# Kernel tuning notes

Measured on AMD Instinct MI355X. Metric: run time of the kernel, lower is better.

## Reference

```python
import jax, jax.numpy as jnp
import numpy as np

E = 1024; H = 16; D = E // H; MAX_LEN = 512; B = 4; N = 1024
EPS = 1e-5
NEG_INF = float('-inf')


def layernorm(x, g, b):
    mu = jnp.mean(x, axis=-1, keepdims=True)
    var = jnp.mean((x - mu) ** 2, axis=-1, keepdims=True)
    return (x - mu) * jax.lax.rsqrt(var + EPS) * g + b


def rel_bias(seq_len, rel_pos):
    # rel_pos: (H, MAX_LEN). bias[h,i,j] = rel_pos[h, i-j] if 0<=i-j<MAX_LEN else -inf
    pos = jnp.arange(seq_len)
    rel = pos[:, None] - pos[None, :]                     # (N, N)
    valid = (rel >= 0) & (rel < rel_pos.shape[-1])
    idx = jnp.clip(rel, 0, rel_pos.shape[-1] - 1)
    gathered = rel_pos[:, idx]                            # (H, N, N)
    return jnp.where(valid[None], gathered, NEG_INF)


def setup_inputs() -> dict:
    key = jax.random.key(0)
    ks = jax.random.split(key, 12)
    s = 0.02
    return {
        'x': jax.random.normal(ks[0], (B, N, E), jnp.float32),
        'rel_pos': jax.random.normal(ks[1], (H, MAX_LEN), jnp.float32),
        'in_proj_w': jax.random.normal(ks[2], (3 * E, E), jnp.float32) * s,
        'in_proj_b': jnp.zeros((3 * E,), jnp.float32),
        'out_w': jax.random.normal(ks[3], (E, E), jnp.float32) * s,
        'out_b': jnp.zeros((E,), jnp.float32),
        'w1': jax.random.normal(ks[4], (4 * E, E), jnp.float32) * s,
        'b1': jnp.zeros((4 * E,), jnp.float32),
        'w2': jax.random.normal(ks[5], (E, 4 * E), jnp.float32) * s,
        'b2': jnp.zeros((E,), jnp.float32),
        'ln1_g': jnp.ones((E,), jnp.float32),
        'ln1_b': jnp.zeros((E,), jnp.float32),
        'ln2_g': jnp.ones((E,), jnp.float32),
        'ln2_b': jnp.zeros((E,), jnp.float32),
    }


def reference(x, rel_pos, in_proj_w, in_proj_b, out_w, out_b,
              w1, b1, w2, b2, ln1_g, ln1_b, ln2_g, ln2_b):
    b, n, e = x.shape
    xn = layernorm(x, ln1_g, ln1_b)
    qkv = xn @ in_proj_w.T + in_proj_b                    # (B, N, 3E)
    q, k, v = jnp.split(qkv, 3, axis=-1)
    # (B, N, E) -> (B, H, N, D)
    def heads(t):
        return t.reshape(b, n, H, D).transpose(0, 2, 1, 3)
    q, k, v = heads(q), heads(k), heads(v)
    bias = rel_bias(n, rel_pos)                           # (H, N, N)
    scores = jnp.einsum('bhnd,bhmd->bhnm', q, k) / np.sqrt(D) + bias[None]
    attn = jax.nn.softmax(scores, axis=-1)
    o = jnp.einsum('bhnm,bhmd->bhnd', attn, v)            # (B, H, N, D)
    o = o.transpose(0, 2, 1, 3).reshape(b, n, e)
    x = x + o @ out_w.T + out_b
    xm = layernorm(x, ln2_g, ln2_b)
    h = jax.nn.relu(xm @ w1.T + b1)
    return x + h @ w2.T + b2
```

## Files before the change

kernel.cpp:

```cpp
#include <hip/hip_runtime.h>
#include <math.h>

#define BB 4
#define NN 1024
#define EE 1024
#define HH 16
#define DD 64
#define MAXLEN 512
#define EPS 1e-5f

typedef __attribute__((ext_vector_type(8))) __bf16 bf16x8;
typedef __attribute__((ext_vector_type(4))) float floatx4;
typedef __attribute__((ext_vector_type(8))) unsigned short ushort8;

#define SWAIT(s) asm volatile("s_waitcnt " s ::: "memory")
#define SCHEDBAR() __builtin_amdgcn_sched_barrier(0)

__device__ __forceinline__ unsigned short f2bf(float f) {
    unsigned u = __float_as_uint(f);
    u += 0x7fffu + ((u >> 16) & 1u);
    return (unsigned short)(u >> 16);
}

template <int MAXR>
__device__ __forceinline__ void vm_wait_rt(int rem) {
    if (rem >= MAXR) {
        if constexpr (MAXR <= 0)      SWAIT("vmcnt(0)");
        else if constexpr (MAXR == 1) SWAIT("vmcnt(4)");
        else if constexpr (MAXR == 2) SWAIT("vmcnt(8)");
        else if constexpr (MAXR == 3) SWAIT("vmcnt(12)");
        else if constexpr (MAXR == 4) SWAIT("vmcnt(16)");
        else if constexpr (MAXR == 5) SWAIT("vmcnt(20)");
        else                          SWAIT("vmcnt(24)");
        return;
    }
    if (rem <= 0) { SWAIT("vmcnt(0)"); return; }
    if (rem == 1) { SWAIT("vmcnt(4)"); return; }
    if constexpr (MAXR >= 3) { if (rem == 2) { SWAIT("vmcnt(8)");  return; } }
    if constexpr (MAXR >= 4) { if (rem == 3) { SWAIT("vmcnt(12)"); return; } }
    if constexpr (MAXR >= 5) { if (rem == 4) { SWAIT("vmcnt(16)"); return; } }
    if constexpr (MAXR >= 6) { if (rem == 5) { SWAIT("vmcnt(20)"); return; } }
}

__global__ __launch_bounds__(256) void f2bf_kernel(const float* __restrict__ in,
                                                   unsigned short* __restrict__ out,
                                                   int n4) {
    int i = blockIdx.x * 256 + threadIdx.x;
    if (i < n4) {
        float4 v = ((const float4*)in)[i];
        ushort4 o;
        o.x = f2bf(v.x); o.y = f2bf(v.y); o.z = f2bf(v.z); o.w = f2bf(v.w);
        ((ushort4*)out)[i] = o;
    }
}

__global__ __launch_bounds__(256) void ln_kernel(const float* __restrict__ x,
                                                 const float* __restrict__ g,
                                                 const float* __restrict__ b,
                                                 unsigned short* __restrict__ out) {
    const int row = blockIdx.x;
    const float* xr = x + (size_t)row * EE;
    float s = 0.f, s2 = 0.f;
    for (int j = threadIdx.x; j < EE; j += 256) {
        float v = xr[j];
        s += v; s2 += v * v;
    }
    for (int off = 32; off > 0; off >>= 1) {
        s  += __shfl_xor(s, off);
        s2 += __shfl_xor(s2, off);
    }
    __shared__ float red[8];
    const int wave = threadIdx.x >> 6, lane = threadIdx.x & 63;
    if (lane == 0) { red[wave] = s; red[4 + wave] = s2; }
    __syncthreads();
    s  = red[0] + red[1] + red[2] + red[3];
    s2 = red[4] + red[5] + red[6] + red[7];
    const float mu  = s * (1.0f / EE);
    const float var = s2 * (1.0f / EE) - mu * mu;
    const float inv = rsqrtf(var + EPS);
    unsigned short* orow = out + (size_t)row * EE;
    for (int j = threadIdx.x; j < EE; j += 256) {
        orow[j] = f2bf((xr[j] - mu) * inv * g[j] + b[j]);
    }
}

template <int BM, int BN, int WMG, int WNG, int DEPTH, int VARIANT, bool XSWZ>
__global__ __launch_bounds__(WMG * WNG * 64, (WMG * WNG == 8) ? 2 : 1)
void gemm_pl_kernel(
    const unsigned short* __restrict__ A,
    const unsigned short* __restrict__ W,
    const float* __restrict__ bias,
    const float* res, void* Cout, int Nc, int K) {
    constexpr int NW  = WMG * WNG;
    constexpr int WTM = BM / WMG;
    constexpr int WTN = BN / WNG;
    constexpr int MR  = WTM / 16;
    constexpr int NR  = WTN / 16;
    static_assert(NR == 4, "NR must be 4");
    constexpr int SA = BM / (16 * NW);
    constexpr int SB = BN / (16 * NW);
    static_assert(SA == 2 && SB == 2, "stage count must be 2+2");
    static_assert((DEPTH & (DEPTH - 1)) == 0, "DEPTH must be pow2");
    constexpr int DMASK = DEPTH - 1;

    __shared__ unsigned short smem[DEPTH][(BM + BN) * 32];

    const int tid  = threadIdx.x;
    const int lane = tid & 63;
    const int wv   = tid >> 6;
    const int wm   = wv / WNG;
    const int wn   = wv % WNG;

    int bx = blockIdx.x, by = blockIdx.y;
    if (XSWZ) {
        const int gx  = gridDim.x;
        const int nwg = gx * gridDim.y;
        const int lin = by * gx + bx;
        const int sl  = (lin & 7) * (nwg >> 3) + (lin >> 3);
        bx = sl % gx; by = sl / gx;
    }
    const int row0 = by * BM;
    const int col0 = bx * BN;
    const int NT   = K >> 5;

    const int srow = lane >> 2;
    const int sq   = ((lane & 3) ^ ((lane >> 3) & 3)) * 8;
    const unsigned short* Ag = A + (size_t)(row0 + srow) * K + sq;
    const unsigned short* Wg = W + (size_t)(col0 + srow) * K + sq;

    auto stage = [&](int t) {
        unsigned short* dst = &smem[t & DMASK][0];
#pragma unroll
        for (int s = 0; s < SA; ++s) {
            const int r = (wv + s * NW) * 16;
            __builtin_amdgcn_global_load_lds(
                (const __attribute__((address_space(1))) unsigned int*)(Ag + (size_t)r * K + t * 32),
                (__attribute__((address_space(3))) unsigned int*)(dst + r * 32), 16, 0, 0);
        }
#pragma unroll
        for (int s = 0; s < SB; ++s) {
            const int r = (wv + s * NW) * 16;
            __builtin_amdgcn_global_load_lds(
                (const __attribute__((address_space(1))) unsigned int*)(Wg + (size_t)r * K + t * 32),
                (__attribute__((address_space(3))) unsigned int*)(dst + (BM + r) * 32), 16, 0, 0);
        }
    };

    const int frow = lane & 15;
    const int quad = lane >> 4;
    const int rq   = (quad ^ ((frow >> 1) & 3)) * 8;
    const int abase = (wm * WTM + frow) * 32 + rq;
    const int bbase = (BM + wn * WTN + frow) * 32 + rq;

    floatx4 acc[MR][4];
#pragma unroll
    for (int m = 0; m < MR; ++m)
#pragma unroll
        for (int n = 0; n < 4; ++n) acc[m][n] = (floatx4){0.f, 0.f, 0.f, 0.f};

    bf16x8 afA[MR], afB[MR];

#pragma unroll
    for (int pt = 0; pt < DEPTH - 1; ++pt) stage(pt);
    vm_wait_rt<DEPTH - 2>(DEPTH - 2);
    __builtin_amdgcn_s_barrier();
    SCHEDBAR();
#pragma unroll
    for (int m = 0; m < MR; ++m)
        afA[m] = *(const bf16x8*)(&smem[0][0] + abase + m * (16 * 32));

#define GEMM_BODY(T, AFC, AFN, TAIL)                                           \
    {                                                                          \
        const int t_ = (T);                                                    \
        if (!(TAIL)) vm_wait_rt<DEPTH - 2>(NT - 2 - t_);                       \
        __builtin_amdgcn_s_barrier();                                          \
        SCHEDBAR();                                                            \
        if (t_ + DEPTH - 1 < NT) stage(t_ + DEPTH - 1);                        \
        const unsigned short* buf_ = &smem[t_ & DMASK][0];                     \
        bf16x8 bfr0 = *(const bf16x8*)(buf_ + bbase);                          \
        bf16x8 bfr1 = *(const bf16x8*)(buf_ + bbase + 16 * 32);                \
        SCHEDBAR();                                                            \
        bf16x8 bfr2 = *(const bf16x8*)(buf_ + bbase + 32 * 32);                \
        bf16x8 bfr3 = *(const bf16x8*)(buf_ + bbase + 48 * 32);                \
        if (!(TAIL)) {                                                         \
            const unsigned short* nbuf_ = &smem[(t_ + 1) & DMASK][0];          \
            _Pragma("unroll")                                                  \
            for (int m = 0; m < MR; ++m)                                       \
                AFN[m] = *(const bf16x8*)(nbuf_ + abase + m * (16 * 32));      \
        }                                                                      \
        SCHEDBAR();                                                            \
        if (TAIL) { SWAIT("lgkmcnt(2)"); }                                     \
        else { if constexpr (MR == 8) SWAIT("lgkmcnt(10)");                    \
               else SWAIT("lgkmcnt(6)"); }                                     \
        SCHEDBAR();                                                            \
        __builtin_amdgcn_s_setprio(1);                                         \
        _Pragma("unroll")                                                      \
        for (int m = 0; m < MR; ++m) {                                         \
            acc[m][0] = __builtin_amdgcn_mfma_f32_16x16x32_bf16(               \
                AFC[m], bfr0, acc[m][0], 0, 0, 0);                             \
            acc[m][1] = __builtin_amdgcn_mfma_f32_16x16x32_bf16(               \
                AFC[m], bfr1, acc[m][1], 0, 0, 0);                             \
        }                                                                      \
        SCHEDBAR();                                                            \
        if (TAIL) { SWAIT("lgkmcnt(0)"); }                                     \
        else { if constexpr (MR == 8) SWAIT("lgkmcnt(8)");                     \
               else SWAIT("lgkmcnt(4)"); }                                     \
        SCHEDBAR();                                                            \
        _Pragma("unroll")                                                      \
        for (int m = 0; m < MR; ++m) {                                         \
            acc[m][2] = __builtin_amdgcn_mfma_f32_16x16x32_bf16(               \
                AFC[m], bfr2, acc[m][2], 0, 0, 0);                             \
            acc[m][3] = __builtin_amdgcn_mfma_f32_16x16x32_bf16(               \
                AFC[m], bfr3, acc[m][3], 0, 0, 0);                             \
        }                                                                      \
        __builtin_amdgcn_s_setprio(0);                                         \
        SCHEDBAR();                                                            \
    }

    int t = 0;
    for (; t < NT - 2; t += 2) {
        GEMM_BODY(t,     afA, afB, false);
        GEMM_BODY(t + 1, afB, afA, false);
    }
    GEMM_BODY(NT - 2, afA, afB, false);
    GEMM_BODY(NT - 1, afB, afA, true);
#undef GEMM_BODY

    const int crow = (lane >> 4) * 4;
    const int ccol = lane & 15;
#pragma unroll
    for (int n = 0; n < 4; ++n) {
        const int nn = col0 + wn * WTN + n * 16 + ccol;
        const float bv = bias[nn];
#pragma unroll
        for (int m = 0; m < MR; ++m) {
#pragma unroll
            for (int r = 0; r < 4; ++r) {
                const int mm = row0 + wm * WTM + m * 16 + crow + r;
                float v = acc[m][n][r] + bv;
                if (VARIANT == 1) v = fmaxf(v, 0.f);
                if (VARIANT == 2) {
                    ((float*)Cout)[(size_t)mm * Nc + nn] = v + res[(size_t)mm * Nc + nn];
                } else {
                    ((unsigned short*)Cout)[(size_t)mm * Nc + nn] = f2bf(v);
                }
            }
        }
    }
}

__global__ __launch_bounds__(512, 2) void gemm_kh_kernel(
    const unsigned short* __restrict__ A,
    const unsigned short* __restrict__ W,
    const float* __restrict__ bias,
    const float* res, float* Cout, int Nc, int K) {
    __shared__ unsigned short smem[4][16384];

    const int tid  = threadIdx.x;
    const int lane = tid & 63;
    const int wv   = tid >> 6;
    const int wk   = wv >> 2;
    const int wm   = (wv >> 1) & 1;
    const int wn   = wv & 1;

    int bx = blockIdx.x, by = blockIdx.y;
    {
        const int gx  = gridDim.x;
        const int nwg = gx * gridDim.y;
        const int lin = by * gx + bx;
        const int sl  = (lin & 7) * (nwg >> 3) + (lin >> 3);
        bx = sl % gx; by = sl / gx;
    }
    const int row0 = by * 128;
    const int col0 = bx * 128;
    const int NT   = K >> 6;

    const int srow = lane >> 3;
    const int sq   = ((lane & 7) ^ ((lane >> 3) & 7)) * 8;
    const unsigned short* Ag = A + (size_t)(row0 + srow) * K + sq;
    const unsigned short* Wg = W + (size_t)(col0 + srow) * K + sq;

    auto stage = [&](int t) {
        unsigned short* dst = &smem[t & 3][0];
#pragma unroll
        for (int s = 0; s < 2; ++s) {
            const int r = (wv + s * 8) * 8;
            __builtin_amdgcn_global_load_lds(
                (const __attribute__((address_space(1))) unsigned int*)(Ag + (size_t)r * K + t * 64),
                (__attribute__((address_space(3))) unsigned int*)(dst + r * 64), 16, 0, 0);
        }
#pragma unroll
        for (int s = 0; s < 2; ++s) {
            const int r = (wv + s * 8) * 8;
            __builtin_amdgcn_global_load_lds(
                (const __attribute__((address_space(1))) unsigned int*)(Wg + (size_t)r * K + t * 64),
                (__attribute__((address_space(3))) unsigned int*)(dst + 8192 + r * 64), 16, 0, 0);
        }
    };

    const int frow = lane & 15;
    const int quad = lane >> 4;
    const int phys = ((wk * 4 + quad) ^ (frow & 7)) * 8;
    const int abase = (wm * 64 + frow) * 64 + phys;
    const int bbase = 8192 + (wn * 64 + frow) * 64 + phys;

    floatx4 acc[4][4];
#pragma unroll
    for (int m = 0; m < 4; ++m)
#pragma unroll
        for (int n = 0; n < 4; ++n) acc[m][n] = (floatx4){0.f, 0.f, 0.f, 0.f};

    bf16x8 afA[4], afB[4];

    stage(0); stage(1); stage(2);
    SWAIT("vmcnt(8)");
    __builtin_amdgcn_s_barrier();
    SCHEDBAR();
#pragma unroll
    for (int m = 0; m < 4; ++m)
        afA[m] = *(const bf16x8*)(&smem[0][0] + abase + m * 1024);

#define KH_BODY(T, AFC, AFN, TAIL)                                             \
    {                                                                          \
        const int t_ = (T);                                                    \
        if (!(TAIL)) vm_wait_rt<2>(NT - 2 - t_);                               \
        __builtin_amdgcn_s_barrier();                                          \
        SCHEDBAR();                                                            \
        if (t_ + 3 < NT) stage(t_ + 3);                                        \
        const unsigned short* buf_ = &smem[t_ & 3][0];                         \
        bf16x8 bfr0 = *(const bf16x8*)(buf_ + bbase);                          \
        bf16x8 bfr1 = *(const bf16x8*)(buf_ + bbase + 1024);                   \
        SCHEDBAR();                                                            \
        bf16x8 bfr2 = *(const bf16x8*)(buf_ + bbase + 2048);                   \
        bf16x8 bfr3 = *(const bf16x8*)(buf_ + bbase + 3072);                   \
        if (!(TAIL)) {                                                         \
            const unsigned short* nbuf_ = &smem[(t_ + 1) & 3][0];              \
            _Pragma("unroll")                                                  \
            for (int m = 0; m < 4; ++m)                                        \
                AFN[m] = *(const bf16x8*)(nbuf_ + abase + m * 1024);           \
        }                                                                      \
        SCHEDBAR();                                                            \
        if (TAIL) { SWAIT("lgkmcnt(2)"); } else { SWAIT("lgkmcnt(6)"); }       \
        SCHEDBAR();                                                            \
        __builtin_amdgcn_s_setprio(1);                                         \
        _Pragma("unroll")                                                      \
        for (int m = 0; m < 4; ++m) {                                          \
            acc[m][0] = __builtin_amdgcn_mfma_f32_16x16x32_bf16(               \
                AFC[m], bfr0, acc[m][0], 0, 0, 0);                             \
            acc[m][1] = __builtin_amdgcn_mfma_f32_16x16x32_bf16(               \
                AFC[m], bfr1, acc[m][1], 0, 0, 0);                             \
        }                                                                      \
        SCHEDBAR();                                                            \
        if (TAIL) { SWAIT("lgkmcnt(0)"); } else { SWAIT("lgkmcnt(4)"); }       \
        SCHEDBAR();                                                            \
        _Pragma("unroll")                                                      \
        for (int m = 0; m < 4; ++m) {                                          \
            acc[m][2] = __builtin_amdgcn_mfma_f32_16x16x32_bf16(               \
                AFC[m], bfr2, acc[m][2], 0, 0, 0);                             \
            acc[m][3] = __builtin_amdgcn_mfma_f32_16x16x32_bf16(               \
                AFC[m], bfr3, acc[m][3], 0, 0, 0);                             \
        }                                                                      \
        __builtin_amdgcn_s_setprio(0);                                         \
        SCHEDBAR();                                                            \
    }

    int t = 0;
    for (; t < NT - 2; t += 2) {
        KH_BODY(t,     afA, afB, false);
        KH_BODY(t + 1, afB, afA, false);
    }
    KH_BODY(NT - 2, afA, afB, false);
    KH_BODY(NT - 1, afB, afA, true);
#undef KH_BODY

    __syncthreads();
    float* pbuf = (float*)&smem[0][0];
    const int pair = wm * 2 + wn;
    if (wk == 1) {
#pragma unroll
        for (int m = 0; m < 4; ++m)
#pragma unroll
            for (int n = 0; n < 4; ++n)
                *(floatx4*)&pbuf[pair * 4096 + (m * 4 + n) * 256 + lane * 4] = acc[m][n];
    }
    __syncthreads();
    if (wk == 0) {
        const int crow = (lane >> 4) * 4;
        const int ccol = lane & 15;
#pragma unroll
        for (int n = 0; n < 4; ++n) {
            const int nn = col0 + wn * 64 + n * 16 + ccol;
            const float bv = bias[nn];
#pragma unroll
            for (int m = 0; m < 4; ++m) {
                floatx4 p = *(const floatx4*)&pbuf[pair * 4096 + (m * 4 + n) * 256 + lane * 4];
#pragma unroll
                for (int r = 0; r < 4; ++r) {
                    const int mm = row0 + wm * 64 + m * 16 + crow + r;
                    Cout[(size_t)mm * Nc + nn] =
                        acc[m][n][r] + p[r] + bv + res[(size_t)mm * Nc + nn];
                }
            }
        }
    }
}

__global__ __launch_bounds__(256) void attn_mfma_kernel(
    const unsigned short* __restrict__ qkv,
    const float* __restrict__ rel_pos,
    unsigned short* __restrict__ o) {
    __shared__ unsigned short K_s[2][64][32];
    __shared__ unsigned short V_s[64][72];
    __shared__ unsigned short P_s[4][2][16][32];
    __shared__ float rel_s[MAXLEN];

    const int qt = blockIdx.x, h = blockIdx.y, b = blockIdx.z;
    const int q0 = qt * 64;
    const int tid  = threadIdx.x;
    const int lane = tid & 63;
    const int w    = tid >> 6;
    const int quad = lane >> 4;
    const int c15  = lane & 15;

    rel_s[tid]       = rel_pos[h * MAXLEN + tid];
    rel_s[tid + 256] = rel_pos[h * MAXLEN + tid + 256];

    const size_t rowstride = 3 * EE;
    const size_t base_q = (size_t)(b * NN) * rowstride + h * DD;
    const size_t base_k = base_q + EE;
    const size_t base_v = base_q + 2 * EE;

    bf16x8 aq[2];
    {
        const unsigned short* qrow =
            qkv + base_q + (size_t)(q0 + w * 16 + c15) * rowstride + quad * 8;
        aq[0] = *(const bf16x8*)(qrow);
        aq[1] = *(const bf16x8*)(qrow + 32);
    }

    floatx4 Oacc[4];
#pragma unroll
    for (int j = 0; j < 4; ++j) Oacc[j] = (floatx4){0.f, 0.f, 0.f, 0.f};
    float m_r[4], l_r[4];
#pragma unroll
    for (int r = 0; r < 4; ++r) { m_r[r] = -1e30f; l_r[r] = 0.f; }

    const int jlo = max(0, q0 - (MAXLEN - 1));
    const int c0 = jlo >> 6;
    const int c1 = (q0 + 63) >> 6;

    for (int cc = c0; cc <= c1; ++cc) {
        const int jb0 = cc << 6;
        __syncthreads();

        {
            const int krow = w * 16 + (lane >> 2);
            const int dofs = (lane & 3) * 8;
            const unsigned short* gk =
                qkv + base_k + (size_t)(jb0 + krow) * rowstride + dofs;
            __builtin_amdgcn_global_load_lds(
                (const __attribute__((address_space(1))) unsigned int*)gk,
                (__attribute__((address_space(3))) unsigned int*)&K_s[0][w * 16][0],
                16, 0, 0);
            __builtin_amdgcn_global_load_lds(
                (const __attribute__((address_space(1))) unsigned int*)(gk + 32),
                (__attribute__((address_space(3))) unsigned int*)&K_s[1][w * 16][0],
                16, 0, 0);
        }
        {
            const int key = lane;
            const int d0  = w * 16;
            const unsigned short* gv =
                qkv + base_v + (size_t)(jb0 + key) * rowstride + d0;
            ushort8 va = *(const ushort8*)(gv);
            ushort8 vb = *(const ushort8*)(gv + 8);
#pragma unroll
            for (int ii = 0; ii < 8; ++ii) V_s[d0 + ii][key] = va[ii];
#pragma unroll
            for (int ii = 0; ii < 8; ++ii) V_s[d0 + 8 + ii][key] = vb[ii];
        }
        __syncthreads();

        floatx4 S[4];
#pragma unroll
        for (int jb = 0; jb < 4; ++jb) {
            S[jb] = (floatx4){0.f, 0.f, 0.f, 0.f};
            bf16x8 bk0 = *(const bf16x8*)&K_s[0][jb * 16 + c15][quad * 8];
            bf16x8 bk1 = *(const bf16x8*)&K_s[1][jb * 16 + c15][quad * 8];
            S[jb] = __builtin_amdgcn_mfma_f32_16x16x32_bf16(aq[0], bk0, S[jb], 0, 0, 0);
            S[jb] = __builtin_amdgcn_mfma_f32_16x16x32_bf16(aq[1], bk1, S[jb], 0, 0, 0);
        }

        const int i_base = q0 + w * 16 + quad * 4;
        float sv[4][4];
        float mc[4] = {-1e30f, -1e30f, -1e30f, -1e30f};
#pragma unroll
        for (int jb = 0; jb < 4; ++jb) {
            const int jg = jb0 + jb * 16 + c15;
#pragma unroll
            for (int r = 0; r < 4; ++r) {
                const int rel = (i_base + r) - jg;
                float s;
                if (rel >= 0 && rel < MAXLEN) s = S[jb][r] * 0.125f + rel_s[rel];
                else                          s = -1e30f;
                sv[jb][r] = s;
                mc[r] = fmaxf(mc[r], s);
            }
        }
#pragma unroll
        for (int off = 1; off < 16; off <<= 1)
#pragma unroll
            for (int r = 0; r < 4; ++r) mc[r] = fmaxf(mc[r], __shfl_xor(mc[r], off));

        float alpha[4], psum[4];
#pragma unroll
        for (int r = 0; r < 4; ++r) {
            const float mn = fmaxf(m_r[r], mc[r]);
            alpha[r] = __expf(m_r[r] - mn);
            m_r[r] = mn;
            psum[r] = 0.f;
        }
#pragma unroll
        for (int jb = 0; jb < 4; ++jb)
#pragma unroll
            for (int r = 0; r < 4; ++r) {
                const float p = __expf(sv[jb][r] - m_r[r]);
                sv[jb][r] = p;
                psum[r] += p;
            }
#pragma unroll
        for (int off = 1; off < 16; off <<= 1)
#pragma unroll
            for (int r = 0; r < 4; ++r) psum[r] += __shfl_xor(psum[r], off);
#pragma unroll
        for (int r = 0; r < 4; ++r) l_r[r] = l_r[r] * alpha[r] + psum[r];
#pragma unroll
        for (int jb = 0; jb < 4; ++jb)
#pragma unroll
            for (int r = 0; r < 4; ++r) Oacc[jb][r] *= alpha[r];

#pragma unroll
        for (int jb = 0; jb < 4; ++jb)
#pragma unroll
            for (int r = 0; r < 4; ++r)
                P_s[w][jb >> 1][quad * 4 + r][(jb & 1) * 16 + c15] = f2bf(sv[jb][r]);

        bf16x8 ap0 = *(const bf16x8*)&P_s[w][0][c15][quad * 8];
        bf16x8 ap1 = *(const bf16x8*)&P_s[w][1][c15][quad * 8];

#pragma unroll
        for (int jd = 0; jd < 4; ++jd) {
            bf16x8 bv0 = *(const bf16x8*)&V_s[jd * 16 + c15][quad * 8];
            bf16x8 bv1 = *(const bf16x8*)&V_s[jd * 16 + c15][32 + quad * 8];
            Oacc[jd] = __builtin_amdgcn_mfma_f32_16x16x32_bf16(ap0, bv0, Oacc[jd], 0, 0, 0);
            Oacc[jd] = __builtin_amdgcn_mfma_f32_16x16x32_bf16(ap1, bv1, Oacc[jd], 0, 0, 0);
        }
    }

    float inv[4];
#pragma unroll
    for (int r = 0; r < 4; ++r) inv[r] = 1.0f / l_r[r];
#pragma unroll
    for (int jd = 0; jd < 4; ++jd) {
#pragma unroll
        for (int r = 0; r < 4; ++r) {
            const int row = q0 + w * 16 + quad * 4 + r;
            const int col = h * DD + jd * 16 + c15;
            o[(size_t)(b * NN + row) * EE + col] = f2bf(Oacc[jd][r] * inv[r]);
        }
    }
}

extern "C" void kernel_launch(void* const* d_in, const int* in_sizes, int n_in,
                              void* d_out, int out_size, void* d_ws, size_t ws_size,
                              hipStream_t stream) {
    const float* x         = (const float*)d_in[0];
    const float* rel_pos   = (const float*)d_in[1];
    const float* in_proj_w = (const float*)d_in[2];
    const float* in_proj_b = (const float*)d_in[3];
    const float* out_w     = (const float*)d_in[4];
    const float* out_b     = (const float*)d_in[5];
    const float* w1        = (const float*)d_in[6];
    const float* b1        = (const float*)d_in[7];
    const float* w2        = (const float*)d_in[8];
    const float* b2        = (const float*)d_in[9];
    const float* ln1_g     = (const float*)d_in[10];
    const float* ln1_b     = (const float*)d_in[11];
    const float* ln2_g     = (const float*)d_in[12];
    const float* ln2_b     = (const float*)d_in[13];
    float* out = (float*)d_out;

    char* wsb = (char*)d_ws;
    const size_t MB = 1024 * 1024;
    unsigned short* wqkv_b = (unsigned short*)(wsb + 0);
    unsigned short* wout_b = (unsigned short*)(wsb + 6 * MB);
    unsigned short* w1_b   = (unsigned short*)(wsb + 8 * MB);
    unsigned short* w2_b   = (unsigned short*)(wsb + 16 * MB);
    unsigned short* xn_b   = (unsigned short*)(wsb + 24 * MB);
    unsigned short* qkv_b  = (unsigned short*)(wsb + 32 * MB);
    unsigned short* h_b    = (unsigned short*)(wsb + 32 * MB);
    unsigned short* o_b    = (unsigned short*)(wsb + 56 * MB);

    const int Mrows = BB * NN;

    f2bf_kernel<<<(3 * EE * EE / 4 + 255) / 256, 256, 0, stream>>>(in_proj_w, wqkv_b, 3 * EE * EE / 4);
    f2bf_kernel<<<(EE * EE / 4 + 255) / 256, 256, 0, stream>>>(out_w, wout_b, EE * EE / 4);
    f2bf_kernel<<<(4 * EE * EE / 4 + 255) / 256, 256, 0, stream>>>(w1, w1_b, 4 * EE * EE / 4);
    f2bf_kernel<<<(4 * EE * EE / 4 + 255) / 256, 256, 0, stream>>>(w2, w2_b, 4 * EE * EE / 4);

    ln_kernel<<<Mrows, 256, 0, stream>>>(x, ln1_g, ln1_b, xn_b);
    gemm_pl_kernel<256, 256, 2, 4, 4, 0, true><<<dim3(3 * EE / 256, Mrows / 256), 512, 0, stream>>>(
        xn_b, wqkv_b, in_proj_b, nullptr, qkv_b, 3 * EE, EE);
    attn_mfma_kernel<<<dim3(NN / 64, HH, BB), 256, 0, stream>>>(qkv_b, rel_pos, o_b);
    gemm_kh_kernel<<<dim3(EE / 128, Mrows / 128), 512, 0, stream>>>(
        o_b, wout_b, out_b, x, out, EE, EE);
    ln_kernel<<<Mrows, 256, 0, stream>>>(out, ln2_g, ln2_b, xn_b);
    gemm_pl_kernel<256, 256, 2, 4, 4, 1, true><<<dim3(4 * EE / 256, Mrows / 256), 512, 0, stream>>>(
        xn_b, w1_b, b1, nullptr, h_b, 4 * EE, EE);
    gemm_kh_kernel<<<dim3(EE / 128, Mrows / 128), 512, 0, stream>>>(
        h_b, w2_b, b2, out, out, EE, 4 * EE);
}
```

Baseline: 340.0 us.

## Replace 256x256 deep-pipelined GEMM with 128x128 double-buffered GEMM; fuse weight casts

Swaps the 256x256, 4-deep pipelined GEMM used for the QKV and FFN1 projections for a simpler 128x128 tile kernel. The new kernel uses 4 waves, double buffering and 3 blocks per CU, which raises the block count and occupancy at the cost of less data reuse per tile and less latency hiding. The four fp32-to-bf16 weight cast launches are merged into one kernel. LayerNorm is vectorised to one float4 per thread.

```diff
diff --git a/kernel.cpp b/kernel.cpp
--- a/kernel.cpp
+++ b/kernel.cpp
@@ -28,30 +28,32 @@
         if constexpr (MAXR <= 0)      SWAIT("vmcnt(0)");
         else if constexpr (MAXR == 1) SWAIT("vmcnt(4)");
         else if constexpr (MAXR == 2) SWAIT("vmcnt(8)");
-        else if constexpr (MAXR == 3) SWAIT("vmcnt(12)");
-        else if constexpr (MAXR == 4) SWAIT("vmcnt(16)");
-        else if constexpr (MAXR == 5) SWAIT("vmcnt(20)");
-        else                          SWAIT("vmcnt(24)");
+        else                          SWAIT("vmcnt(12)");
         return;
     }
     if (rem <= 0) { SWAIT("vmcnt(0)"); return; }
     if (rem == 1) { SWAIT("vmcnt(4)"); return; }
     if constexpr (MAXR >= 3) { if (rem == 2) { SWAIT("vmcnt(8)");  return; } }
-    if constexpr (MAXR >= 4) { if (rem == 3) { SWAIT("vmcnt(12)"); return; } }
-    if constexpr (MAXR >= 5) { if (rem == 4) { SWAIT("vmcnt(16)"); return; } }
-    if constexpr (MAXR >= 6) { if (rem == 5) { SWAIT("vmcnt(20)"); return; } }
-}
-
-__global__ __launch_bounds__(256) void f2bf_kernel(const float* __restrict__ in,
-                                                   unsigned short* __restrict__ out,
-                                                   int n4) {
+}
+
+__global__ __launch_bounds__(256) void f2bf_all_kernel(
+    const float* __restrict__ s0, const float* __restrict__ s1,
+    const float* __restrict__ s2, const float* __restrict__ s3,
+    unsigned short* __restrict__ d0, unsigned short* __restrict__ d1,
+    unsigned short* __restrict__ d2, unsigned short* __restrict__ d3) {
+    const int C0 = 3 * EE * EE / 4;
+    const int C1 = C0 + EE * EE / 4;
+    const int C2 = C1 + EE * EE;
     int i = blockIdx.x * 256 + threadIdx.x;
-    if (i < n4) {
-        float4 v = ((const float4*)in)[i];
-        ushort4 o;
-        o.x = f2bf(v.x); o.y = f2bf(v.y); o.z = f2bf(v.z); o.w = f2bf(v.w);
-        ((ushort4*)out)[i] = o;
-    }
+    const float* in; unsigned short* out; int j;
+    if (i < C0)      { in = s0; out = d0; j = i; }
+    else if (i < C1) { in = s1; out = d1; j = i - C0; }
+    else if (i < C2) { in = s2; out = d2; j = i - C1; }
+    else             { in = s3; out = d3; j = i - C2; }
+    float4 v = ((const float4*)in)[j];
+    ushort4 o;
+    o.x = f2bf(v.x); o.y = f2bf(v.y); o.z = f2bf(v.z); o.w = f2bf(v.w);
+    ((ushort4*)out)[j] = o;
 }
 
 __global__ __launch_bounds__(256) void ln_kernel(const float* __restrict__ x,
@@ -59,18 +61,16 @@
                                                  const float* __restrict__ b,
                                                  unsigned short* __restrict__ out) {
     const int row = blockIdx.x;
-    const float* xr = x + (size_t)row * EE;
-    float s = 0.f, s2 = 0.f;
-    for (int j = threadIdx.x; j < EE; j += 256) {
-        float v = xr[j];
-        s += v; s2 += v * v;
-    }
+    const int tid = threadIdx.x;
+    const float4 v = ((const float4*)(x + (size_t)row * EE))[tid];
+    float s  = v.x + v.y + v.z + v.w;
+    float s2 = v.x * v.x + v.y * v.y + v.z * v.z + v.w * v.w;
     for (int off = 32; off > 0; off >>= 1) {
         s  += __shfl_xor(s, off);
         s2 += __shfl_xor(s2, off);
     }
     __shared__ float red[8];
-    const int wave = threadIdx.x >> 6, lane = threadIdx.x & 63;
+    const int wave = tid >> 6, lane = tid & 63;
     if (lane == 0) { red[wave] = s; red[4 + wave] = s2; }
     __syncthreads();
     s  = red[0] + red[1] + red[2] + red[3];
@@ -78,49 +78,40 @@
     const float mu  = s * (1.0f / EE);
     const float var = s2 * (1.0f / EE) - mu * mu;
     const float inv = rsqrtf(var + EPS);
-    unsigned short* orow = out + (size_t)row * EE;
-    for (int j = threadIdx.x; j < EE; j += 256) {
-        orow[j] = f2bf((xr[j] - mu) * inv * g[j] + b[j]);
-    }
-}
-
-template <int BM, int BN, int WMG, int WNG, int DEPTH, int VARIANT, bool XSWZ>
-__global__ __launch_bounds__(WMG * WNG * 64, (WMG * WNG == 8) ? 2 : 1)
-void gemm_pl_kernel(
+    const float4 gv = ((const float4*)g)[tid];
+    const float4 bv = ((const float4*)b)[tid];
+    ushort4 o;
+    o.x = f2bf((v.x - mu) * inv * gv.x + bv.x);
+    o.y = f2bf((v.y - mu) * inv * gv.y + bv.y);
+    o.z = f2bf((v.z - mu) * inv * gv.z + bv.z);
+    o.w = f2bf((v.w - mu) * inv * gv.w + bv.w);
+    ((ushort4*)(out + (size_t)row * EE))[tid] = o;
+}
+
+template <int VARIANT>
+__global__ __launch_bounds__(256, 3) void gemm97t_kernel(
     const unsigned short* __restrict__ A,
     const unsigned short* __restrict__ W,
     const float* __restrict__ bias,
-    const float* res, void* Cout, int Nc, int K) {
-    constexpr int NW  = WMG * WNG;
-    constexpr int WTM = BM / WMG;
-    constexpr int WTN = BN / WNG;
-    constexpr int MR  = WTM / 16;
-    constexpr int NR  = WTN / 16;
-    static_assert(NR == 4, "NR must be 4");
-    constexpr int SA = BM / (16 * NW);
-    constexpr int SB = BN / (16 * NW);
-    static_assert(SA == 2 && SB == 2, "stage count must be 2+2");
-    static_assert((DEPTH & (DEPTH - 1)) == 0, "DEPTH must be pow2");
-    constexpr int DMASK = DEPTH - 1;
-
-    __shared__ unsigned short smem[DEPTH][(BM + BN) * 32];
+    void* __restrict__ Cout, int Nc, int K) {
+    __shared__ unsigned short smem[2][8192];
 
     const int tid  = threadIdx.x;
     const int lane = tid & 63;
     const int wv   = tid >> 6;
-    const int wm   = wv / WNG;
-    const int wn   = wv % WNG;
+    const int wm   = wv >> 1;
+    const int wn   = wv & 1;
 
     int bx = blockIdx.x, by = blockIdx.y;
-    if (XSWZ) {
+    {
         const int gx  = gridDim.x;
         const int nwg = gx * gridDim.y;
         const int lin = by * gx + bx;
         const int sl  = (lin & 7) * (nwg >> 3) + (lin >> 3);
         bx = sl % gx; by = sl / gx;
     }
-    const int row0 = by * BM;
-    const int col0 = bx * BN;
+    const int row0 = by * 128;
+    const int col0 = bx * 128;
     const int NT   = K >> 5;
 
     const int srow = lane >> 2;
@@ -129,121 +120,92 @@
     const unsigned short* Wg = W + (size_t)(col0 + srow) * K + sq;
 
     auto stage = [&](int t) {
-        unsigned short* dst = &smem[t & DMASK][0];
-#pragma unroll
-        for (int s = 0; s < SA; ++s) {
-            const int r = (wv + s * NW) * 16;
+        unsigned short* dst = &smem[t & 1][0];
+#pragma unroll
+        for (int s = 0; s < 2; ++s) {
+            const int r = (wv + s * 4) * 16;
             __builtin_amdgcn_global_load_lds(
                 (const __attribute__((address_space(1))) unsigned int*)(Ag + (size_t)r * K + t * 32),
                 (__attribute__((address_space(3))) unsigned int*)(dst + r * 32), 16, 0, 0);
         }
 #pragma unroll
-        for (int s = 0; s < SB; ++s) {
-            const int r = (wv + s * NW) * 16;
+        for (int s = 0; s < 2; ++s) {
+            const int r = (wv + s * 4) * 16;
             __builtin_amdgcn_global_load_lds(
                 (const __attribute__((address_space(1))) unsigned int*)(Wg + (size_t)r * K + t * 32),
-                (__attribute__((address_space(3))) unsigned int*)(dst + (BM + r) * 32), 16, 0, 0);
+                (__attribute__((address_space(3))) unsigned int*)(dst + 4096 + r * 32), 16, 0, 0);
         }
     };
 
     const int frow = lane & 15;
     const int quad = lane >> 4;
     const int rq   = (quad ^ ((frow >> 1) & 3)) * 8;
-    const int abase = (wm * WTM + frow) * 32 + rq;
-    const int bbase = (BM + wn * WTN + frow) * 32 + rq;
-
-    floatx4 acc[MR][4];
-#pragma unroll
-    for (int m = 0; m < MR; ++m)
+    const int abase = (wm * 64 + frow) * 32 + rq;
+    const int bbase = 4096 + (wn * 64 + frow) * 32 + rq;
+
+    floatx4 acc[4][4];
+#pragma unroll
+    for (int m = 0; m < 4; ++m)
 #pragma unroll
         for (int n = 0; n < 4; ++n) acc[m][n] = (floatx4){0.f, 0.f, 0.f, 0.f};
 
-    bf16x8 afA[MR], afB[MR];
-
-#pragma unroll
-    for (int pt = 0; pt < DEPTH - 1; ++pt) stage(pt);
-    vm_wait_rt<DEPTH - 2>(DEPTH - 2);
-    __builtin_amdgcn_s_barrier();
-    SCHEDBAR();
-#pragma unroll
-    for (int m = 0; m < MR; ++m)
-        afA[m] = *(const bf16x8*)(&smem[0][0] + abase + m * (16 * 32));
-
-#define GEMM_BODY(T, AFC, AFN, TAIL)                                           \
-    {                                                                          \
-        const int t_ = (T);                                                    \
-        if (!(TAIL)) vm_wait_rt<DEPTH - 2>(NT - 2 - t_);                       \
-        __builtin_amdgcn_s_barrier();                                          \
-        SCHEDBAR();                                                            \
-        if (t_ + DEPTH - 1 < NT) stage(t_ + DEPTH - 1);                        \
-        const unsigned short* buf_ = &smem[t_ & DMASK][0];                     \
-        bf16x8 bfr0 = *(const bf16x8*)(buf_ + bbase);                          \
-        bf16x8 bfr1 = *(const bf16x8*)(buf_ + bbase + 16 * 32);                \
-        SCHEDBAR();                                                            \
-        bf16x8 bfr2 = *(const bf16x8*)(buf_ + bbase + 32 * 32);                \
-        bf16x8 bfr3 = *(const bf16x8*)(buf_ + bbase + 48 * 32);                \
-        if (!(TAIL)) {                                                         \
-            const unsigned short* nbuf_ = &smem[(t_ + 1) & DMASK][0];          \
-            _Pragma("unroll")                                                  \
-            for (int m = 0; m < MR; ++m)                                       \
-                AFN[m] = *(const bf16x8*)(nbuf_ + abase + m * (16 * 32));      \
-        }                                                                      \
-        SCHEDBAR();                                                            \
-        if (TAIL) { SWAIT("lgkmcnt(2)"); }                                     \
-        else { if constexpr (MR == 8) SWAIT("lgkmcnt(10)");                    \
-               else SWAIT("lgkmcnt(6)"); }                                     \
-        SCHEDBAR();                                                            \
-        __builtin_amdgcn_s_setprio(1);                                         \
-        _Pragma("unroll")                                                      \
-        for (int m = 0; m < MR; ++m) {                                         \
-            acc[m][0] = __builtin_amdgcn_mfma_f32_16x16x32_bf16(               \
-                AFC[m], bfr0, acc[m][0], 0, 0, 0);                             \
-            acc[m][1] = __builtin_amdgcn_mfma_f32_16x16x32_bf16(               \
-                AFC[m], bfr1, acc[m][1], 0, 0, 0);                             \
-        }                                                                      \
-        SCHEDBAR();                                                            \
-        if (TAIL) { SWAIT("lgkmcnt(0)"); }                                     \
-        else { if constexpr (MR == 8) SWAIT("lgkmcnt(8)");                     \
-               else SWAIT("lgkmcnt(4)"); }                                     \
-        SCHEDBAR();                                                            \
-        _Pragma("unroll")                                                      \
-        for (int m = 0; m < MR; ++m) {                                         \
-            acc[m][2] = __builtin_amdgcn_mfma_f32_16x16x32_bf16(               \
-                AFC[m], bfr2, acc[m][2], 0, 0, 0);                             \
-            acc[m][3] = __builtin_amdgcn_mfma_f32_16x16x32_bf16(               \
-                AFC[m], bfr3, acc[m][3], 0, 0, 0);                             \
-        }                                                                      \
-        __builtin_amdgcn_s_setprio(0);                                         \
-        SCHEDBAR();                                                            \
-    }
-
-    int t = 0;
-    for (; t < NT - 2; t += 2) {
-        GEMM_BODY(t,     afA, afB, false);
-        GEMM_BODY(t + 1, afB, afA, false);
-    }
-    GEMM_BODY(NT - 2, afA, afB, false);
-    GEMM_BODY(NT - 1, afB, afA, true);
-#undef GEMM_BODY
-
+    stage(0); stage(1);
+
+    for (int t = 0; t < NT; ++t) {
+        if (t == NT - 1) { SWAIT("vmcnt(0)"); } else { SWAIT("vmcnt(4)"); }
+        __builtin_amdgcn_s_barrier();
+        SCHEDBAR();
+
+        const unsigned short* buf = &smem[t & 1][0];
+        bf16x8 af0 = *(const bf16x8*)(buf + abase);
+        bf16x8 af1 = *(const bf16x8*)(buf + abase + 512);
+        bf16x8 af2 = *(const bf16x8*)(buf + abase + 1024);
+        bf16x8 af3 = *(const bf16x8*)(buf + abase + 1536);
+        bf16x8 bf0 = *(const bf16x8*)(buf + bbase);
+        bf16x8 bf1 = *(const bf16x8*)(buf + bbase + 512);
+        bf16x8 bf2 = *(const bf16x8*)(buf + bbase + 1024);
+        bf16x8 bf3 = *(const bf16x8*)(buf + bbase + 1536);
+
+        __builtin_amdgcn_s_setprio(1);
+#pragma unroll
+        for (int m = 0; m < 4; ++m)
+            acc[m][0] = __builtin_amdgcn_mfma_f32_16x16x32_bf16(
+                (m == 0 ? af0 : m == 1 ? af1 : m == 2 ? af2 : af3), bf0, acc[m][0], 0, 0, 0);
+#pragma unroll
+        for (int m = 0; m < 4; ++m)
+            acc[m][1] = __builtin_amdgcn_mfma_f32_16x16x32_bf16(
+                (m == 0 ? af0 : m == 1 ? af1 : m == 2 ? af2 : af3), bf1, acc[m][1], 0, 0, 0);
+#pragma unroll
+        for (int m = 0; m < 4; ++m)
+            acc[m][2] = __builtin_amdgcn_mfma_f32_16x16x32_bf16(
+                (m == 0 ? af0 : m == 1 ? af1 : m == 2 ? af2 : af3), bf2, acc[m][2], 0, 0, 0);
+#pragma unroll
+        for (int m = 0; m < 4; ++m)
+            acc[m][3] = __builtin_amdgcn_mfma_f32_16x16x32_bf16(
+                (m == 0 ? af0 : m == 1 ? af1 : m == 2 ? af2 : af3), bf3, acc[m][3], 0, 0, 0);
+        __builtin_amdgcn_s_setprio(0);
+        SCHEDBAR();
+        __builtin_amdgcn_s_barrier();
+        SCHEDBAR();
+        if (t + 2 < NT) stage(t + 2);
+        SCHEDBAR();
+    }
+
+    unsigned short* Cb = (unsigned short*)Cout;
     const int crow = (lane >> 4) * 4;
     const int ccol = lane & 15;
 #pragma unroll
     for (int n = 0; n < 4; ++n) {
-        const int nn = col0 + wn * WTN + n * 16 + ccol;
+        const int nn = col0 + wn * 64 + n * 16 + ccol;
         const float bv = bias[nn];
 #pragma unroll
-        for (int m = 0; m < MR; ++m) {
+        for (int m = 0; m < 4; ++m) {
 #pragma unroll
             for (int r = 0; r < 4; ++r) {
-                const int mm = row0 + wm * WTM + m * 16 + crow + r;
+                const int mm = row0 + wm * 64 + m * 16 + crow + r;
                 float v = acc[m][n][r] + bv;
                 if (VARIANT == 1) v = fmaxf(v, 0.f);
-                if (VARIANT == 2) {
-                    ((float*)Cout)[(size_t)mm * Nc + nn] = v + res[(size_t)mm * Nc + nn];
-                } else {
-                    ((unsigned short*)Cout)[(size_t)mm * Nc + nn] = f2bf(v);
-                }
+                Cb[(size_t)mm * Nc + nn] = f2bf(v);
             }
         }
     }
@@ -603,20 +565,18 @@
 
     const int Mrows = BB * NN;
 
-    f2bf_kernel<<<(3 * EE * EE / 4 + 255) / 256, 256, 0, stream>>>(in_proj_w, wqkv_b, 3 * EE * EE / 4);
-    f2bf_kernel<<<(EE * EE / 4 + 255) / 256, 256, 0, stream>>>(out_w, wout_b, EE * EE / 4);
-    f2bf_kernel<<<(4 * EE * EE / 4 + 255) / 256, 256, 0, stream>>>(w1, w1_b, 4 * EE * EE / 4);
-    f2bf_kernel<<<(4 * EE * EE / 4 + 255) / 256, 256, 0, stream>>>(w2, w2_b, 4 * EE * EE / 4);
+    f2bf_all_kernel<<<3 * EE * EE / 256, 256, 0, stream>>>(
+        in_proj_w, out_w, w1, w2, wqkv_b, wout_b, w1_b, w2_b);
 
     ln_kernel<<<Mrows, 256, 0, stream>>>(x, ln1_g, ln1_b, xn_b);
-    gemm_pl_kernel<256, 256, 2, 4, 4, 0, true><<<dim3(3 * EE / 256, Mrows / 256), 512, 0, stream>>>(
-        xn_b, wqkv_b, in_proj_b, nullptr, qkv_b, 3 * EE, EE);
+    gemm97t_kernel<0><<<dim3(3 * EE / 128, Mrows / 128), 256, 0, stream>>>(
+        xn_b, wqkv_b, in_proj_b, qkv_b, 3 * EE, EE);
     attn_mfma_kernel<<<dim3(NN / 64, HH, BB), 256, 0, stream>>>(qkv_b, rel_pos, o_b);
     gemm_kh_kernel<<<dim3(EE / 128, Mrows / 128), 512, 0, stream>>>(
         o_b, wout_b, out_b, x, out, EE, EE);
     ln_kernel<<<Mrows, 256, 0, stream>>>(out, ln2_g, ln2_b, xn_b);
-    gemm_pl_kernel<256, 256, 2, 4, 4, 1, true><<<dim3(4 * EE / 256, Mrows / 256), 512, 0, stream>>>(
-        xn_b, w1_b, b1, nullptr, h_b, 4 * EE, EE);
+    gemm97t_kernel<1><<<dim3(4 * EE / 128, Mrows / 128), 256, 0, stream>>>(
+        xn_b, w1_b, b1, h_b, 4 * EE, EE);
     gemm_kh_kernel<<<dim3(EE / 128, Mrows / 128), 512, 0, stream>>>(
         h_b, w2_b, b2, out, out, EE, 4 * EE);
 }
```

Result: faster. 327.8 us (-3.6%).
